# Performance work log

Measured on AMD Instinct MI355X. Metric: run time of the kernel, lower is better.

The kernel has to match this reference:

```python
import jax, jax.numpy as jnp
import numpy as np

B_, C_, H_, W_ = 32, 128, 64, 64


def setup_inputs() -> dict:
    key = jax.random.key(0)
    ks = jax.random.split(key, 7)
    s = 1.0 / np.sqrt(C_)
    return {
        "input": jax.random.normal(ks[0], (B_, C_, H_, W_), dtype=jnp.float32),
        "wA": jax.random.normal(ks[1], (C_, C_), dtype=jnp.float32) * s,
        "bA": jax.random.normal(ks[2], (C_,), dtype=jnp.float32) * 0.01,
        "wB": jax.random.normal(ks[3], (C_, C_), dtype=jnp.float32) * s,
        "bB": jax.random.normal(ks[4], (C_,), dtype=jnp.float32) * 0.01,
        "wV": jax.random.normal(ks[5], (C_, C_), dtype=jnp.float32) * s,
        "bV": jax.random.normal(ks[6], (C_,), dtype=jnp.float32) * 0.01,
    }


def reference(input, wA, bA, wB, bB, wV, bV):
    b, c, h, w = input.shape
    hw = h * w
    x = input.reshape(b, c, hw)  # 1x1 conv == channel matmul over flattened spatial
    A = jnp.einsum('oc,bcn->bon', wA, x) + bA[None, :, None]  # (b,c,hw)
    Bm = jnp.einsum('oc,bcn->bon', wB, x) + bB[None, :, None]
    V = jnp.einsum('oc,bcn->bon', wV, x) + bV[None, :, None]
    sm_B = jax.nn.softmax(Bm, axis=-1)  # softmax over spatial per channel
    # global_descriptors[b,i,j] = mean_hw(A[b,j,:] * sm_B[b,i,:]) -> GEMM, no (b,c,c,hw) tensor
    gd = jnp.einsum('bin,bjn->bij', sm_B, A) / hw  # (b,c,c)
    av = jax.nn.softmax(V, axis=-1)  # (b,c,hw)
    # out[b,j,n] = sum_i av[b,i,n] * gd[b,i,j]  (bmm(av^T, gd) then transpose back)
    out = jnp.einsum('bin,bij->bjn', av, gd)
    return out.reshape(b, c, h, w)
```

## Files before the change

kernel.cpp:

```cpp
#include <hip/hip_runtime.h>
#include <hip/hip_bf16.h>


#define B_  32
#define C_  128
#define HW_ 4096

typedef __attribute__((ext_vector_type(8))) __bf16 bf16x8;
typedef __attribute__((ext_vector_type(4))) float f32x4;

__device__ __forceinline__ unsigned int bf_rne(float f) {
    unsigned int u = __float_as_uint(f);
    return (u + 0x7fffu + ((u >> 16) & 1u)) >> 16;
}
__device__ __forceinline__ float bf_hi(float f) {
    unsigned int u = __float_as_uint(f);
    return __uint_as_float((u + 0x7fffu + ((u >> 16) & 1u)) & 0xffff0000u);
}

__global__ __launch_bounds__(256) void k0_prep(
    const float* __restrict__ wB, const float* __restrict__ wV,
    unsigned short* __restrict__ Wh, unsigned short* __restrict__ Wl)
{
    int g = blockIdx.x * 256 + threadIdx.x;
    int row = g >> 5, c4 = (g & 31) << 2;
    const float* src = (row < 128) ? &wB[row * 128] : &wV[(row - 128) * 128];
    float4 v = *(const float4*)&src[c4];
    float vv[4] = {v.x, v.y, v.z, v.w};
    unsigned int h[4], l[4];
#pragma unroll
    for (int e = 0; e < 4; ++e) {
        float hf = bf_hi(vv[e]);
        h[e] = __float_as_uint(hf) >> 16;
        l[e] = bf_rne(vv[e] - hf);
    }
    *(uint2*)&Wh[row * 128 + c4] = make_uint2(h[0] | (h[1] << 16), h[2] | (h[3] << 16));
    *(uint2*)&Wl[row * 128 + c4] = make_uint2(l[0] | (l[1] << 16), l[2] | (l[3] << 16));
}

__global__ __launch_bounds__(1024, 1) void k1_fused(
    const float* __restrict__ x,
    const unsigned short* __restrict__ Wh, const unsigned short* __restrict__ Wl,
    const float* __restrict__ bB, const float* __restrict__ bV,
    unsigned short* __restrict__ expVT, float* __restrict__ T_part,
    float* __restrict__ Zcat)
{
    __shared__ unsigned short XT_h[32 * 136];
    __shared__ unsigned short XT_l[32 * 136];
    __shared__ unsigned short XN_h[128 * 40];
    __shared__ unsigned short XN_l[128 * 40];
    __shared__ unsigned short EBs[128 * 40];
    __shared__ unsigned short EVs[32 * 136];
    __shared__ float bias_s[256];

    const int t = threadIdx.x;
    const int lane = t & 63, w = t >> 6;
    const int col16 = lane & 15, quad = lane >> 4;
    const int b = blockIdx.y;
    const int n0 = blockIdx.x * 256;
    const float* xb = x + (size_t)b * C_ * HW_;

    const int snA = t & 31, cq0 = t >> 5;
    const int scB = t >> 3, sqB = (t & 7) * 4;

    const int rowbase = w * 16;
    const int lbase = (w & 7) * 16;
    const int boff = (w < 8) ? 0 : 128;
    const int mh = (w >> 3) * 64;
    const int nh = (w & 7) * 16;

    if (t < 256) bias_s[t] = (t < 128) ? bB[t] : bV[t - 128];

    f32x4 tacc[4];
    float zacc[4];
#pragma unroll
    for (int i = 0; i < 4; ++i) { tacc[i] = (f32x4){0.f,0.f,0.f,0.f}; zacc[i] = 0.f; }

    float xrA[4], xrB[4];
#pragma unroll
    for (int cc = 0; cc < 4; ++cc)
        xrA[cc] = xb[(size_t)(cq0 * 4 + cc) * HW_ + n0 + snA];
    *(float4*)xrB = *(const float4*)&xb[(size_t)scB * HW_ + n0 + sqB];

    for (int st = 0; st < 8; ++st) {
        unsigned int ha[4], la[4];
#pragma unroll
        for (int e = 0; e < 4; ++e) {
            float hf = bf_hi(xrA[e]);
            ha[e] = __float_as_uint(hf) >> 16;
            la[e] = bf_rne(xrA[e] - hf);
        }
        __syncthreads();
        *(uint2*)&XT_h[snA * 136 + cq0 * 4] = make_uint2(ha[0] | (ha[1] << 16), ha[2] | (ha[3] << 16));
        *(uint2*)&XT_l[snA * 136 + cq0 * 4] = make_uint2(la[0] | (la[1] << 16), la[2] | (la[3] << 16));
        {
            unsigned int hb[4], lb[4];
#pragma unroll
            for (int e = 0; e < 4; ++e) {
                float hf = bf_hi(xrB[e]);
                hb[e] = __float_as_uint(hf) >> 16;
                lb[e] = bf_rne(xrB[e] - hf);
            }
            *(uint2*)&XN_h[scB * 40 + sqB] = make_uint2(hb[0] | (hb[1] << 16), hb[2] | (hb[3] << 16));
            *(uint2*)&XN_l[scB * 40 + sqB] = make_uint2(lb[0] | (lb[1] << 16), lb[2] | (lb[3] << 16));
        }
        __syncthreads();
        if (st < 7) {
            int ns2 = n0 + (st + 1) * 32;
#pragma unroll
            for (int cc = 0; cc < 4; ++cc)
                xrA[cc] = xb[(size_t)(cq0 * 4 + cc) * HW_ + ns2 + snA];
            *(float4*)xrB = *(const float4*)&xb[(size_t)scB * HW_ + ns2 + sqB];
        }

        f32x4 e0 = (f32x4){0.f,0.f,0.f,0.f}, e1 = (f32x4){0.f,0.f,0.f,0.f};
#pragma unroll
        for (int ks = 0; ks < 4; ++ks) {
            int kc = ks * 32 + quad * 8;
            bf16x8 xh0 = *(const bf16x8*)&XT_h[col16 * 136 + kc];
            bf16x8 xl0 = *(const bf16x8*)&XT_l[col16 * 136 + kc];
            bf16x8 xh1 = *(const bf16x8*)&XT_h[(16 + col16) * 136 + kc];
            bf16x8 xl1 = *(const bf16x8*)&XT_l[(16 + col16) * 136 + kc];
            int row = rowbase + col16;
            bf16x8 wh = *(const bf16x8*)&Wh[row * 128 + kc];
            bf16x8 wl = *(const bf16x8*)&Wl[row * 128 + kc];
            e0 = __builtin_amdgcn_mfma_f32_16x16x32_bf16(wh, xh0, e0, 0, 0, 0);
            e0 = __builtin_amdgcn_mfma_f32_16x16x32_bf16(wh, xl0, e0, 0, 0, 0);
            e0 = __builtin_amdgcn_mfma_f32_16x16x32_bf16(wl, xh0, e0, 0, 0, 0);
            e1 = __builtin_amdgcn_mfma_f32_16x16x32_bf16(wh, xh1, e1, 0, 0, 0);
            e1 = __builtin_amdgcn_mfma_f32_16x16x32_bf16(wh, xl1, e1, 0, 0, 0);
            e1 = __builtin_amdgcn_mfma_f32_16x16x32_bf16(wl, xh1, e1, 0, 0, 0);
        }

#pragma unroll
        for (int r = 0; r < 4; ++r) {
            int lrow = lbase + quad * 4 + r;
            float bb = bias_s[boff + lrow];
            float v0 = __expf(e0[r] + bb);
            float v1 = __expf(e1[r] + bb);
            zacc[r] += v0 + v1;
            if (w < 8) {
                EBs[lrow * 40 + col16]      = (unsigned short)bf_rne(v0);
                EBs[lrow * 40 + 16 + col16] = (unsigned short)bf_rne(v1);
            } else {
                EVs[col16 * 136 + lrow]        = (unsigned short)bf_rne(v0);
                EVs[(16 + col16) * 136 + lrow] = (unsigned short)bf_rne(v1);
            }
        }
        __syncthreads();

        {
            int c = nh + col16;
            bf16x8 bh = *(const bf16x8*)&XN_h[c * 40 + quad * 8];
            bf16x8 bl = *(const bf16x8*)&XN_l[c * 40 + quad * 8];
#pragma unroll
            for (int mt = 0; mt < 4; ++mt) {
                bf16x8 a = *(const bf16x8*)&EBs[(mh + mt * 16 + col16) * 40 + quad * 8];
                tacc[mt] = __builtin_amdgcn_mfma_f32_16x16x32_bf16(a, bh, tacc[mt], 0, 0, 0);
                tacc[mt] = __builtin_amdgcn_mfma_f32_16x16x32_bf16(a, bl, tacc[mt], 0, 0, 0);
            }
        }
        {
            int nl = t >> 5, io = (t & 31) * 4;
            *(uint2*)&expVT[((size_t)b * HW_ + n0 + st * 32 + nl) * 128 + io] =
                *(const uint2*)&EVs[nl * 136 + io];
        }
    }

    float* Tp = T_part + (((size_t)blockIdx.x * B_) + b) * 128 * 128;
#pragma unroll
    for (int mt = 0; mt < 4; ++mt)
#pragma unroll
        for (int r = 0; r < 4; ++r)
            Tp[(mh + mt * 16 + quad * 4 + r) * 128 + nh + col16] = tacc[mt][r];

#pragma unroll
    for (int r = 0; r < 4; ++r) {
        float rs = zacc[r];
        rs += __shfl_xor(rs, 1, 16);
        rs += __shfl_xor(rs, 2, 16);
        rs += __shfl_xor(rs, 4, 16);
        rs += __shfl_xor(rs, 8, 16);
        if (col16 == 0)
            atomicAdd(&Zcat[b * 256 + boff + lbase + quad * 4 + r], rs);
    }
}

__global__ __launch_bounds__(256) void k3b_G(
    const float* __restrict__ T_part, const float* __restrict__ wA,
    const float* __restrict__ bA, const float* __restrict__ Zcat,
    unsigned short* __restrict__ Gth, unsigned short* __restrict__ Gtm, int np)
{
    const int t = threadIdx.x;
    const int tx = t & 15, ty = t >> 4;
    const int b = blockIdx.y;
    const int jb = (blockIdx.x >> 2) * 16;
    const int ib = (blockIdx.x & 3) * 32;

    __shared__ float Ts[32][36];
    __shared__ float Wa[16][36];

    float acc[2] = {0.f, 0.f};

    for (int c0 = 0; c0 < 128; c0 += 32) {
        __syncthreads();
        {
            int r = t >> 3, kq = (t & 7) << 2;
            float4 s = make_float4(0.f, 0.f, 0.f, 0.f);
            for (int p = 0; p < np; ++p) {
                float4 v = *(const float4*)&T_part[(((size_t)p * B_ + b) * 128 + ib + r) * 128 + c0 + kq];
                s.x += v.x; s.y += v.y; s.z += v.z; s.w += v.w;
            }
            *(float4*)&Ts[r][kq] = s;
        }
        if (t < 128) {
            int r = t >> 3, kq = (t & 7) << 2;
            *(float4*)&Wa[r][kq] = *(const float4*)&wA[(jb + r) * 128 + c0 + kq];
        }
        __syncthreads();
#pragma unroll
        for (int k = 0; k < 32; k += 4) {
            float4 wv  = *(const float4*)&Wa[ty][k];
            float4 tv0 = *(const float4*)&Ts[tx][k];
            float4 tv1 = *(const float4*)&Ts[16 + tx][k];
            acc[0] = fmaf(wv.x, tv0.x, acc[0]);
            acc[0] = fmaf(wv.y, tv0.y, acc[0]);
            acc[0] = fmaf(wv.z, tv0.z, acc[0]);
            acc[0] = fmaf(wv.w, tv0.w, acc[0]);
            acc[1] = fmaf(wv.x, tv1.x, acc[1]);
            acc[1] = fmaf(wv.y, tv1.y, acc[1]);
            acc[1] = fmaf(wv.z, tv1.z, acc[1]);
            acc[1] = fmaf(wv.w, tv1.w, acc[1]);
        }
    }
    const float* ZB = Zcat + b * 256;
    const float* ZV = ZB + 128;
    {
        int j = jb + ty;
        float bj = bA[j];
#pragma unroll
        for (int ii = 0; ii < 2; ++ii) {
            int i = ib + ii * 16 + tx;
            float g = (acc[ii] / ZB[i] + bj) / (4096.f * ZV[i]);
            float h = bf_hi(g);  float r1 = g - h;
            float m = bf_hi(r1);
            size_t o = ((size_t)b * 128 + j) * 128 + i;
            Gth[o] = (unsigned short)(__float_as_uint(h) >> 16);
            Gtm[o] = (unsigned short)(__float_as_uint(m) >> 16);
        }
    }
}

__global__ __launch_bounds__(256, 6) void k4_out(
    const unsigned short* __restrict__ expVT,
    const unsigned short* __restrict__ Gth, const unsigned short* __restrict__ Gtm,
    float* __restrict__ out)
{
    __shared__ unsigned short Vs[64 * 136];

    const int t = threadIdx.x;
    const int lane = t & 63, w = t >> 6;
    const int col16 = lane & 15, quad = lane >> 4;
    const int b = blockIdx.y, nb = blockIdx.x * 64;

#pragma unroll
    for (int it = 0; it < 4; ++it) {
        int idx = it * 256 + t;
        int n = idx >> 4, o = idx & 15;
        int o2 = (o + 4 * (n & 3)) & 15;
        *(uint4*)&Vs[n * 136 + o2 * 8] =
            *(const uint4*)&expVT[((size_t)b * HW_ + nb + n) * 128 + o2 * 8];
    }
    __syncthreads();

    f32x4 acc[8];
#pragma unroll
    for (int i = 0; i < 8; ++i) acc[i] = (f32x4){0.f,0.f,0.f,0.f};

    const unsigned short* gh = Gth + (size_t)b * 128 * 128;
    const unsigned short* gm = Gtm + (size_t)b * 128 * 128;

#pragma unroll
    for (int ks = 0; ks < 4; ++ks) {
        int ko = ks * 32 + quad * 8;
        bf16x8 vfr = *(const bf16x8*)&Vs[(w * 16 + col16) * 136 + ko];
#pragma unroll
        for (int mt = 0; mt < 8; ++mt) {
            int j = mt * 16 + col16;
            bf16x8 ah = *(const bf16x8*)&gh[j * 128 + ko];
            bf16x8 am = *(const bf16x8*)&gm[j * 128 + ko];
            acc[mt] = __builtin_amdgcn_mfma_f32_16x16x32_bf16(ah, vfr, acc[mt], 0, 0, 0);
            acc[mt] = __builtin_amdgcn_mfma_f32_16x16x32_bf16(am, vfr, acc[mt], 0, 0, 0);
        }
    }
    float* ob = out + (size_t)b * C_ * HW_;
#pragma unroll
    for (int mt = 0; mt < 8; ++mt)
#pragma unroll
        for (int r = 0; r < 4; ++r) {
            int j = mt * 16 + quad * 4 + r;
            int n = nb + w * 16 + col16;
            ob[(size_t)j * HW_ + n] = acc[mt][r];
        }
}

extern "C" void kernel_launch(void* const* d_in, const int* in_sizes, int n_in,
                              void* d_out, int out_size, void* d_ws, size_t ws_size,
                              hipStream_t stream)
{
    const float* x  = (const float*)d_in[0];
    const float* wA = (const float*)d_in[1];
    const float* bA = (const float*)d_in[2];
    const float* wB = (const float*)d_in[3];
    const float* bB = (const float*)d_in[4];
    const float* wV = (const float*)d_in[5];
    const float* bV = (const float*)d_in[6];
    float* out = (float*)d_out;

    char* ws = (char*)d_ws;
    float*          Zcat  = (float*)ws;
    unsigned short* Wh    = (unsigned short*)(ws + 32768);
    unsigned short* Wl    = (unsigned short*)(ws + 98304);
    unsigned short* expVT = (unsigned short*)(ws + 163840);
    float*          T_part= (float*)(ws + 33718272);
    unsigned short* Gth   = (unsigned short*)(ws + 33718272 + 16 * 2097152);
    unsigned short* Gtm   = Gth + 128 * 128 * 32;

    hipMemsetAsync(Zcat, 0, 32768, stream);

    k0_prep <<<dim3(32),     256,  0, stream>>>(wB, wV, Wh, Wl);
    k1_fused<<<dim3(16, 32), 1024, 0, stream>>>(x, Wh, Wl, bB, bV, expVT, T_part, Zcat);
    k3b_G   <<<dim3(32, 32), 256,  0, stream>>>(T_part, wA, bA, Zcat, Gth, Gtm, 16);
    k4_out  <<<dim3(64, 32), 256,  0, stream>>>(expVT, Gth, Gtm, out);
}
```

Baseline: 253.8 us.

## Stage G in LDS for output GEMM and split partial-T reduction into own kernel

The output kernel now loads the full per-batch G hi/mid matrices into XOR-swizzled LDS once per block. Each block covers 256 spatial columns with 512 threads, each wave handling two n-tiles and reading V fragments directly from global memory. Previously every block re-read G from global memory. Separately, the 16-way partial-T sum moves out of k3b_G into a dedicated reduction kernel, so k3b_G no longer repeats that summation for each j-tile. The trade-offs are an extra launch, an extra 2 MB T buffer round trip, and lower occupancy from 64 KB of LDS per block.

```diff
diff --git a/kernel.cpp b/kernel.cpp
--- a/kernel.cpp
+++ b/kernel.cpp
@@ -186,10 +186,24 @@
     }
 }
 
+__global__ __launch_bounds__(256) void k2b_red(
+    const float* __restrict__ T_part, float* __restrict__ T)
+{
+    int g = blockIdx.x * 256 + threadIdx.x;
+    size_t o = (size_t)g * 4;
+    float4 s = make_float4(0.f, 0.f, 0.f, 0.f);
+#pragma unroll
+    for (int p = 0; p < 16; ++p) {
+        float4 v = *(const float4*)&T_part[(size_t)p * (B_ * 128 * 128) + o];
+        s.x += v.x; s.y += v.y; s.z += v.z; s.w += v.w;
+    }
+    *(float4*)&T[o] = s;
+}
+
 __global__ __launch_bounds__(256) void k3b_G(
-    const float* __restrict__ T_part, const float* __restrict__ wA,
+    const float* __restrict__ T, const float* __restrict__ wA,
     const float* __restrict__ bA, const float* __restrict__ Zcat,
-    unsigned short* __restrict__ Gth, unsigned short* __restrict__ Gtm, int np)
+    unsigned short* __restrict__ Gth, unsigned short* __restrict__ Gtm)
 {
     const int t = threadIdx.x;
     const int tx = t & 15, ty = t >> 4;
@@ -206,12 +220,7 @@
         __syncthreads();
         {
             int r = t >> 3, kq = (t & 7) << 2;
-            float4 s = make_float4(0.f, 0.f, 0.f, 0.f);
-            for (int p = 0; p < np; ++p) {
-                float4 v = *(const float4*)&T_part[(((size_t)p * B_ + b) * 128 + ib + r) * 128 + c0 + kq];
-                s.x += v.x; s.y += v.y; s.z += v.z; s.w += v.w;
-            }
-            *(float4*)&Ts[r][kq] = s;
+            *(float4*)&Ts[r][kq] = *(const float4*)&T[((size_t)b * 128 + ib + r) * 128 + c0 + kq];
         }
         if (t < 128) {
             int r = t >> 3, kq = (t & 7) << 2;
@@ -251,57 +260,70 @@
     }
 }
 
-__global__ __launch_bounds__(256, 6) void k4_out(
+__global__ __launch_bounds__(512, 2) void k4_out(
     const unsigned short* __restrict__ expVT,
     const unsigned short* __restrict__ Gth, const unsigned short* __restrict__ Gtm,
     float* __restrict__ out)
 {
-    __shared__ unsigned short Vs[64 * 136];
+    __shared__ unsigned short Gs_h[128 * 128];
+    __shared__ unsigned short Gs_m[128 * 128];
 
     const int t = threadIdx.x;
     const int lane = t & 63, w = t >> 6;
     const int col16 = lane & 15, quad = lane >> 4;
-    const int b = blockIdx.y, nb = blockIdx.x * 64;
-
-#pragma unroll
-    for (int it = 0; it < 4; ++it) {
-        int idx = it * 256 + t;
-        int n = idx >> 4, o = idx & 15;
-        int o2 = (o + 4 * (n & 3)) & 15;
-        *(uint4*)&Vs[n * 136 + o2 * 8] =
-            *(const uint4*)&expVT[((size_t)b * HW_ + nb + n) * 128 + o2 * 8];
-    }
-    __syncthreads();
-
-    f32x4 acc[8];
-#pragma unroll
-    for (int i = 0; i < 8; ++i) acc[i] = (f32x4){0.f,0.f,0.f,0.f};
+    const int b = blockIdx.y, nb = blockIdx.x * 256;
 
     const unsigned short* gh = Gth + (size_t)b * 128 * 128;
     const unsigned short* gm = Gtm + (size_t)b * 128 * 128;
 
 #pragma unroll
+    for (int it = 0; it < 4; ++it) {
+        int idx = it * 512 + t;
+        int j = idx >> 4, o = idx & 15;
+        int od = (o ^ (j & 15)) << 3;
+        *(uint4*)&Gs_h[j * 128 + od] = *(const uint4*)&gh[j * 128 + (o << 3)];
+        *(uint4*)&Gs_m[j * 128 + od] = *(const uint4*)&gm[j * 128 + (o << 3)];
+    }
+    __syncthreads();
+
+    f32x4 acc[8][2];
+#pragma unroll
+    for (int i = 0; i < 8; ++i)
+#pragma unroll
+        for (int j = 0; j < 2; ++j) acc[i][j] = (f32x4){0.f,0.f,0.f,0.f};
+
+#pragma unroll
     for (int ks = 0; ks < 4; ++ks) {
-        int ko = ks * 32 + quad * 8;
-        bf16x8 vfr = *(const bf16x8*)&Vs[(w * 16 + col16) * 136 + ko];
+        bf16x8 vfr[2];
+#pragma unroll
+        for (int nt = 0; nt < 2; ++nt) {
+            int n = nb + w * 32 + nt * 16 + col16;
+            vfr[nt] = *(const bf16x8*)&expVT[((size_t)b * HW_ + n) * 128 + ks * 32 + quad * 8];
+        }
+        int pc = ((ks * 4 + quad) ^ col16) << 3;
 #pragma unroll
         for (int mt = 0; mt < 8; ++mt) {
             int j = mt * 16 + col16;
-            bf16x8 ah = *(const bf16x8*)&gh[j * 128 + ko];
-            bf16x8 am = *(const bf16x8*)&gm[j * 128 + ko];
-            acc[mt] = __builtin_amdgcn_mfma_f32_16x16x32_bf16(ah, vfr, acc[mt], 0, 0, 0);
-            acc[mt] = __builtin_amdgcn_mfma_f32_16x16x32_bf16(am, vfr, acc[mt], 0, 0, 0);
+            bf16x8 ah = *(const bf16x8*)&Gs_h[j * 128 + pc];
+            bf16x8 am = *(const bf16x8*)&Gs_m[j * 128 + pc];
+#pragma unroll
+            for (int nt = 0; nt < 2; ++nt) {
+                acc[mt][nt] = __builtin_amdgcn_mfma_f32_16x16x32_bf16(ah, vfr[nt], acc[mt][nt], 0, 0, 0);
+                acc[mt][nt] = __builtin_amdgcn_mfma_f32_16x16x32_bf16(am, vfr[nt], acc[mt][nt], 0, 0, 0);
+            }
         }
     }
     float* ob = out + (size_t)b * C_ * HW_;
 #pragma unroll
     for (int mt = 0; mt < 8; ++mt)
 #pragma unroll
-        for (int r = 0; r < 4; ++r) {
-            int j = mt * 16 + quad * 4 + r;
-            int n = nb + w * 16 + col16;
-            ob[(size_t)j * HW_ + n] = acc[mt][r];
-        }
+        for (int nt = 0; nt < 2; ++nt)
+#pragma unroll
+            for (int r = 0; r < 4; ++r) {
+                int j = mt * 16 + quad * 4 + r;
+                int n = nb + w * 32 + nt * 16 + col16;
+                ob[(size_t)j * HW_ + n] = acc[mt][nt][r];
+            }
 }
 
 extern "C" void kernel_launch(void* const* d_in, const int* in_sizes, int n_in,
@@ -323,13 +345,15 @@
     unsigned short* Wl    = (unsigned short*)(ws + 98304);
     unsigned short* expVT = (unsigned short*)(ws + 163840);
     float*          T_part= (float*)(ws + 33718272);
-    unsigned short* Gth   = (unsigned short*)(ws + 33718272 + 16 * 2097152);
+    float*          T     = (float*)(ws + 67272704);
+    unsigned short* Gth   = (unsigned short*)(ws + 69369856);
     unsigned short* Gtm   = Gth + 128 * 128 * 32;
 
     hipMemsetAsync(Zcat, 0, 32768, stream);
 
     k0_prep <<<dim3(32),     256,  0, stream>>>(wB, wV, Wh, Wl);
     k1_fused<<<dim3(16, 32), 1024, 0, stream>>>(x, Wh, Wl, bB, bV, expVT, T_part, Zcat);
-    k3b_G   <<<dim3(32, 32), 256,  0, stream>>>(T_part, wA, bA, Zcat, Gth, Gtm, 16);
-    k4_out  <<<dim3(64, 32), 256,  0, stream>>>(expVT, Gth, Gtm, out);
-}
+    k2b_red <<<dim3(512),    256,  0, stream>>>(T_part, T);
+    k3b_G   <<<dim3(32, 32), 256,  0, stream>>>(T, wA, bA, Zcat, Gth, Gtm);
+    k4_out  <<<dim3(16, 32), 512,  0, stream>>>(expVT, Gth, Gtm, out);
+}
```

After: 208.4 us. -17.9%, faster.
